# Kernel optimization log

Measured on AMD Instinct MI355X. Metric: run time of the kernel, lower is better.

The kernel has to match this reference:

```python
import jax, jax.numpy as jnp
import numpy as np

N, M, D = 131072, 512, 128  # points, codebook size, feature dim


def setup_inputs() -> dict:
    key = jax.random.key(0)
    k1, k2 = jax.random.split(key)
    X = jax.random.normal(k1, (N, D), dtype=jnp.float32)
    samples = jax.random.normal(k2, (M, D), dtype=jnp.float32)
    return {"X": X, "samples": samples}


def reference(X, samples):
    # Pairwise L2 distance: sum((x - s)^2, axis=-1) ** (1/2), vectorized via
    # for p=2, without materializing an [N, M, D] tensor).
    x2 = jnp.sum(X * X, axis=1, keepdims=True)              # [N, 1]
    s2 = jnp.sum(samples * samples, axis=1)[None, :]        # [1, M]
    d2 = x2 + s2 - 2.0 * (X @ samples.T)                    # [N, M]
    m_dis = jnp.sqrt(jnp.maximum(d2, 0.0))                  # [N, M]
    # soft=True branch: softmax over axis=0 (across points), as in the original.
    return jax.nn.softmax(-m_dis, axis=0)
```

## Files before the change

kernel.cpp:

```cpp
#include <hip/hip_runtime.h>
#include <hip/hip_bf16.h>

#define NPTS 131072
#define MCB  512
#define DIM  128
#define NRB  (NPTS/128)
#define NCBK (MCB/128)
#define NBLK (NRB*NCBK)

typedef __attribute__((ext_vector_type(4))) float  f32x4;
typedef __attribute__((ext_vector_type(8))) __bf16 bf16x8;
typedef unsigned short u16;
typedef unsigned int   u32;

__device__ __forceinline__ u32 swz(u32 p) { return p ^ (((p >> 8) & 7u) << 4); }

__global__ __launch_bounds__(256) void convert_rows(const float* __restrict__ in,
                                                    u16* __restrict__ outb,
                                                    float* __restrict__ sq,
                                                    int nrows) {
  int wv = threadIdx.x >> 6, ln = threadIdx.x & 63;
  int half = ln >> 5, li = ln & 31;
  int npairs = nrows >> 1;
  for (int pr = blockIdx.x * 4 + wv; pr < npairs; pr += gridDim.x * 4) {
    int row = pr * 2 + half;
    const float4 v = *(const float4*)(in + (size_t)row * DIM + li * 4);
    __hip_bfloat16 b0 = __float2bfloat16(v.x);
    __hip_bfloat16 b1 = __float2bfloat16(v.y);
    __hip_bfloat16 b2 = __float2bfloat16(v.z);
    __hip_bfloat16 b3 = __float2bfloat16(v.w);
    ushort4 o;
    o.x = *(const u16*)&b0; o.y = *(const u16*)&b1;
    o.z = *(const u16*)&b2; o.w = *(const u16*)&b3;
    *(ushort4*)(outb + (size_t)row * DIM + li * 4) = o;
    float f0 = __bfloat162float(b0), f1 = __bfloat162float(b1);
    float f2 = __bfloat162float(b2), f3 = __bfloat162float(b3);
    float s = f0 * f0 + f1 * f1 + f2 * f2 + f3 * f3;
    s += __shfl_xor(s, 1); s += __shfl_xor(s, 2); s += __shfl_xor(s, 4);
    s += __shfl_xor(s, 8); s += __shfl_xor(s, 16);
    if (li == 0) sq[row] = s;
  }
}

template <int WRITE>
__global__ __launch_bounds__(256, 3) void gemm_pass(const u16* __restrict__ Xb,
                                                    const u16* __restrict__ Sb,
                                                    const float* __restrict__ x2,
                                                    const float* __restrict__ s2,
                                                    const float* __restrict__ invs,
                                                    float* __restrict__ outp) {
  __shared__ u16 Bt[128 * DIM];
  __shared__ float lx2[128], ls2[128], lscale[128];
  __shared__ float colsum2[4][64];

  int t = threadIdx.x, wv = t >> 6, ln = t & 63;
  u32 h = blockIdx.x;
  u32 l = (h & 7u) * (NBLK / 8) + (h >> 3);
  u32 rb = l >> 2, cb = l & 3u;
  u32 n0 = rb * 128, m0 = cb * 128;

  const char* Bg = (const char*)(Sb + (size_t)m0 * DIM);
#pragma unroll
  for (int i = 0; i < 8; i++) {
    u32 lb = (u32)(i * 4 + wv) * 1024u;
    u32 go = swz(lb + (u32)ln * 16u);
    __builtin_amdgcn_global_load_lds((const __attribute__((address_space(1))) void*)(Bg + go),
                                     (__attribute__((address_space(3))) void*)((char*)Bt + lb),
                                     16, 0, 0);
  }

  int wr = wv >> 1, wc = wv & 1;
  int rbw = wr * 64, cbw = wc * 64;
  int lr = ln & 15, lg = ln >> 4;

  bf16x8 af[4][4];
  const u16* Abase = Xb + (size_t)(n0 + rbw) * DIM;
#pragma unroll
  for (int i = 0; i < 4; i++)
#pragma unroll
    for (int kk = 0; kk < 4; kk++)
      af[i][kk] = *(const bf16x8*)(Abase + (i * 16 + lr) * DIM + kk * 32 + lg * 8);

  if (t < 128) {
    lx2[t] = x2[n0 + t];
    ls2[t] = s2[m0 + t];
    if (WRITE) lscale[t] = invs[m0 + t];
  }
  __syncthreads();

  f32x4 acc[4][4];
#pragma unroll
  for (int i = 0; i < 4; i++)
#pragma unroll
    for (int j = 0; j < 4; j++) acc[i][j] = (f32x4){0.f, 0.f, 0.f, 0.f};

#pragma unroll
  for (int kk = 0; kk < 4; kk++) {
    bf16x8 bfr[4];
#pragma unroll
    for (int j = 0; j < 4; j++)
      bfr[j] = *(const bf16x8*)((const char*)Bt +
               swz((u32)((cbw + j * 16 + lr) * 256 + kk * 64 + lg * 16)));
#pragma unroll
    for (int i = 0; i < 4; i++)
#pragma unroll
      for (int j = 0; j < 4; j++) {
        if (WRITE)
          acc[i][j] = __builtin_amdgcn_mfma_f32_16x16x32_bf16(bfr[j], af[i][kk], acc[i][j], 0, 0, 0);
        else
          acc[i][j] = __builtin_amdgcn_mfma_f32_16x16x32_bf16(af[i][kk], bfr[j], acc[i][j], 0, 0, 0);
      }
  }

  if (WRITE) {
#pragma unroll
    for (int i = 0; i < 4; i++) {
      int n = rbw + i * 16 + lr;
      float xx = lx2[n];
      float* orow = outp + (size_t)(n0 + n) * MCB + m0;
#pragma unroll
      for (int j = 0; j < 4; j++) {
        int mb = cbw + j * 16 + lg * 4;
        f32x4 v;
#pragma unroll
        for (int r = 0; r < 4; r++) {
          float d2 = xx + ls2[mb + r] - 2.f * acc[i][j][r];
          d2 = fmaxf(d2, 0.f);
          float e = __expf(-__fsqrt_rn(d2));
          v[r] = e * lscale[mb + r];
        }
        __builtin_nontemporal_store(v, (f32x4*)(orow + mb));
      }
    }
  } else {
    float csum[4] = {0.f, 0.f, 0.f, 0.f};
#pragma unroll
    for (int i = 0; i < 4; i++) {
#pragma unroll
      for (int j = 0; j < 4; j++) {
        int m = cbw + j * 16 + lr;
        float ss = ls2[m];
#pragma unroll
        for (int r = 0; r < 4; r++) {
          int n = rbw + i * 16 + lg * 4 + r;
          float d2 = lx2[n] + ss - 2.f * acc[i][j][r];
          d2 = fmaxf(d2, 0.f);
          csum[j] += __expf(-__fsqrt_rn(d2));
        }
      }
    }
#pragma unroll
    for (int j = 0; j < 4; j++) {
      float v = csum[j];
      v += __shfl_xor(v, 16);
      v += __shfl_xor(v, 32);
      if (ln < 16) colsum2[wv][j * 16 + ln] = v;
    }
    __syncthreads();
    if (t < 128) {
      int wcf = t >> 6, lc = t & 63;
      outp[(size_t)rb * MCB + m0 + t] = colsum2[wcf][lc] + colsum2[wcf + 2][lc];
    }
  }
}

__global__ __launch_bounds__(256) void reduce_cols(const float* __restrict__ partial,
                                                   float* __restrict__ invs) {
  int m = blockIdx.x, t = threadIdx.x;
  float s = 0.f;
  for (int k = t; k < NRB; k += 256) s += partial[(size_t)k * MCB + m];
  s += __shfl_xor(s, 1);  s += __shfl_xor(s, 2);  s += __shfl_xor(s, 4);
  s += __shfl_xor(s, 8);  s += __shfl_xor(s, 16); s += __shfl_xor(s, 32);
  __shared__ float w4[4];
  if ((t & 63) == 0) w4[t >> 6] = s;
  __syncthreads();
  if (t == 0) invs[m] = 1.0f / (w4[0] + w4[1] + w4[2] + w4[3]);
}

extern "C" void kernel_launch(void* const* d_in, const int* in_sizes, int n_in,
                              void* d_out, int out_size, void* d_ws, size_t ws_size,
                              hipStream_t stream) {
  const float* X = (const float*)d_in[0];
  const float* S = (const float*)d_in[1];
  float* out = (float*)d_out;
  char* ws = (char*)d_ws;

  u16*   Xb      = (u16*)ws;
  u16*   Sb      = (u16*)(ws + 33554432);
  float* x2      = (float*)(ws + 33685504);
  float* s2      = (float*)(ws + 34209792);
  float* invs    = (float*)(ws + 34211840);
  float* partial = (float*)(ws + 34213888);

  convert_rows<<<2048, 256, 0, stream>>>(X, Xb, x2, NPTS);
  convert_rows<<<64, 256, 0, stream>>>(S, Sb, s2, MCB);
  gemm_pass<0><<<NBLK, 256, 0, stream>>>(Xb, Sb, x2, s2, invs, partial);
  reduce_cols<<<MCB, 256, 0, stream>>>(partial, invs);
  gemm_pass<1><<<NBLK, 256, 0, stream>>>(Xb, Sb, x2, s2, invs, out);
}
```

Baseline: 398.3 us.

## Fuse X conversion into pass1 and loop codebook tiles per row block

Folds the X fp32-to-bf16 conversion and row-norm computation into the first GEMM pass, so each block converts its own 128 rows and then reuses them from registers. Each block now iterates over all four 128-column codebook tiles instead of launching one block per tile. This cuts the number of blocks and avoids reloading the A fragments per tile. B fragments now come straight from global/L2 rather than from swizzled LDS, and reduce_cols handles 8 columns per block for coalesced reads. The risks are lower parallelism (1024 blocks), longer per-block serial work, and uncached B loads.

New measurement: 426.6 us. +7.1%, slower.

```diff
diff --git a/kernel.cpp b/kernel.cpp
--- a/kernel.cpp
+++ b/kernel.cpp
@@ -4,16 +4,12 @@
 #define NPTS 131072
 #define MCB  512
 #define DIM  128
-#define NRB  (NPTS/128)
-#define NCBK (MCB/128)
-#define NBLK (NRB*NCBK)
+#define NRB  1024
 
 typedef __attribute__((ext_vector_type(4))) float  f32x4;
 typedef __attribute__((ext_vector_type(8))) __bf16 bf16x8;
 typedef unsigned short u16;
 typedef unsigned int   u32;
-
-__device__ __forceinline__ u32 swz(u32 p) { return p ^ (((p >> 8) & 7u) << 4); }
 
 __global__ __launch_bounds__(256) void convert_rows(const float* __restrict__ in,
                                                     u16* __restrict__ outb,
@@ -42,113 +38,97 @@
   }
 }
 
-template <int WRITE>
-__global__ __launch_bounds__(256, 3) void gemm_pass(const u16* __restrict__ Xb,
-                                                    const u16* __restrict__ Sb,
-                                                    const float* __restrict__ x2,
-                                                    const float* __restrict__ s2,
-                                                    const float* __restrict__ invs,
-                                                    float* __restrict__ outp) {
-  __shared__ u16 Bt[128 * DIM];
-  __shared__ float lx2[128], ls2[128], lscale[128];
+__global__ __launch_bounds__(256, 2) void pass1(const float* __restrict__ X,
+                                                const u16* __restrict__ Sb,
+                                                const float* __restrict__ s2,
+                                                u16* __restrict__ Xb,
+                                                float* __restrict__ x2,
+                                                float* __restrict__ partial) {
   __shared__ float colsum2[4][64];
-
   int t = threadIdx.x, wv = t >> 6, ln = t & 63;
   u32 h = blockIdx.x;
-  u32 l = (h & 7u) * (NBLK / 8) + (h >> 3);
-  u32 rb = l >> 2, cb = l & 3u;
-  u32 n0 = rb * 128, m0 = cb * 128;
-
-  const char* Bg = (const char*)(Sb + (size_t)m0 * DIM);
-#pragma unroll
-  for (int i = 0; i < 8; i++) {
-    u32 lb = (u32)(i * 4 + wv) * 1024u;
-    u32 go = swz(lb + (u32)ln * 16u);
-    __builtin_amdgcn_global_load_lds((const __attribute__((address_space(1))) void*)(Bg + go),
-                                     (__attribute__((address_space(3))) void*)((char*)Bt + lb),
-                                     16, 0, 0);
-  }
+  u32 rb = (h & 7u) * (NRB / 8) + (h >> 3);
+  u32 n0 = rb * 128;
+
+  {
+    int half = ln >> 5, li = ln & 31;
+    const float* Xblk = X + (size_t)n0 * DIM;
+    u16* Xbblk = Xb + (size_t)n0 * DIM;
+#pragma unroll
+    for (int it = 0; it < 16; ++it) {
+      int row = (it * 4 + wv) * 2 + half;
+      const float4 v = *(const float4*)(Xblk + (size_t)row * DIM + li * 4);
+      __hip_bfloat16 b0 = __float2bfloat16(v.x);
+      __hip_bfloat16 b1 = __float2bfloat16(v.y);
+      __hip_bfloat16 b2 = __float2bfloat16(v.z);
+      __hip_bfloat16 b3 = __float2bfloat16(v.w);
+      ushort4 o;
+      o.x = *(const u16*)&b0; o.y = *(const u16*)&b1;
+      o.z = *(const u16*)&b2; o.w = *(const u16*)&b3;
+      *(ushort4*)(Xbblk + (size_t)row * DIM + li * 4) = o;
+      float f0 = __bfloat162float(b0), f1 = __bfloat162float(b1);
+      float f2 = __bfloat162float(b2), f3 = __bfloat162float(b3);
+      float s = f0 * f0 + f1 * f1 + f2 * f2 + f3 * f3;
+      s += __shfl_xor(s, 1); s += __shfl_xor(s, 2); s += __shfl_xor(s, 4);
+      s += __shfl_xor(s, 8); s += __shfl_xor(s, 16);
+      if (li == 0) x2[n0 + row] = s;
+    }
+  }
+  __syncthreads();
 
   int wr = wv >> 1, wc = wv & 1;
   int rbw = wr * 64, cbw = wc * 64;
   int lr = ln & 15, lg = ln >> 4;
 
   bf16x8 af[4][4];
-  const u16* Abase = Xb + (size_t)(n0 + rbw) * DIM;
+  const u16* Ab = Xb + (size_t)(n0 + rbw) * DIM;
 #pragma unroll
   for (int i = 0; i < 4; i++)
 #pragma unroll
     for (int kk = 0; kk < 4; kk++)
-      af[i][kk] = *(const bf16x8*)(Abase + (i * 16 + lr) * DIM + kk * 32 + lg * 8);
-
-  if (t < 128) {
-    lx2[t] = x2[n0 + t];
-    ls2[t] = s2[m0 + t];
-    if (WRITE) lscale[t] = invs[m0 + t];
-  }
-  __syncthreads();
-
-  f32x4 acc[4][4];
+      af[i][kk] = *(const bf16x8*)(Ab + (i * 16 + lr) * DIM + kk * 32 + lg * 8);
+
+  f32x4 lxv[4];
 #pragma unroll
   for (int i = 0; i < 4; i++)
-#pragma unroll
-    for (int j = 0; j < 4; j++) acc[i][j] = (f32x4){0.f, 0.f, 0.f, 0.f};
-
-#pragma unroll
-  for (int kk = 0; kk < 4; kk++) {
-    bf16x8 bfr[4];
-#pragma unroll
-    for (int j = 0; j < 4; j++)
-      bfr[j] = *(const bf16x8*)((const char*)Bt +
-               swz((u32)((cbw + j * 16 + lr) * 256 + kk * 64 + lg * 16)));
+    lxv[i] = *(const f32x4*)(x2 + n0 + rbw + i * 16 + lg * 4);
+
+#pragma unroll
+  for (int cb = 0; cb < 4; ++cb) {
+    int m0c = cb * 128;
+    f32x4 acc[4][4];
 #pragma unroll
     for (int i = 0; i < 4; i++)
 #pragma unroll
-      for (int j = 0; j < 4; j++) {
-        if (WRITE)
-          acc[i][j] = __builtin_amdgcn_mfma_f32_16x16x32_bf16(bfr[j], af[i][kk], acc[i][j], 0, 0, 0);
-        else
-          acc[i][j] = __builtin_amdgcn_mfma_f32_16x16x32_bf16(af[i][kk], bfr[j], acc[i][j], 0, 0, 0);
-      }
-  }
-
-  if (WRITE) {
-#pragma unroll
-    for (int i = 0; i < 4; i++) {
-      int n = rbw + i * 16 + lr;
-      float xx = lx2[n];
-      float* orow = outp + (size_t)(n0 + n) * MCB + m0;
-#pragma unroll
-      for (int j = 0; j < 4; j++) {
-        int mb = cbw + j * 16 + lg * 4;
-        f32x4 v;
+      for (int j = 0; j < 4; j++) acc[i][j] = (f32x4){0.f, 0.f, 0.f, 0.f};
+
+#pragma unroll
+    for (int kk = 0; kk < 4; kk++) {
+      bf16x8 bb[4];
+#pragma unroll
+      for (int j = 0; j < 4; j++)
+        bb[j] = *(const bf16x8*)(Sb + (size_t)(m0c + cbw + j * 16 + lr) * DIM + kk * 32 + lg * 8);
+#pragma unroll
+      for (int i = 0; i < 4; i++)
+#pragma unroll
+        for (int j = 0; j < 4; j++)
+          acc[i][j] = __builtin_amdgcn_mfma_f32_16x16x32_bf16(af[i][kk], bb[j], acc[i][j], 0, 0, 0);
+    }
+
+    float s2v[4];
+#pragma unroll
+    for (int j = 0; j < 4; j++) s2v[j] = s2[m0c + cbw + j * 16 + lr];
+    float csum[4] = {0.f, 0.f, 0.f, 0.f};
+#pragma unroll
+    for (int i = 0; i < 4; i++)
+#pragma unroll
+      for (int j = 0; j < 4; j++)
 #pragma unroll
         for (int r = 0; r < 4; r++) {
-          float d2 = xx + ls2[mb + r] - 2.f * acc[i][j][r];
-          d2 = fmaxf(d2, 0.f);
-          float e = __expf(-__fsqrt_rn(d2));
-          v[r] = e * lscale[mb + r];
-        }
-        __builtin_nontemporal_store(v, (f32x4*)(orow + mb));
-      }
-    }
-  } else {
-    float csum[4] = {0.f, 0.f, 0.f, 0.f};
-#pragma unroll
-    for (int i = 0; i < 4; i++) {
-#pragma unroll
-      for (int j = 0; j < 4; j++) {
-        int m = cbw + j * 16 + lr;
-        float ss = ls2[m];
-#pragma unroll
-        for (int r = 0; r < 4; r++) {
-          int n = rbw + i * 16 + lg * 4 + r;
-          float d2 = lx2[n] + ss - 2.f * acc[i][j][r];
+          float d2 = lxv[i][r] + s2v[j] - 2.f * acc[i][j][r];
           d2 = fmaxf(d2, 0.f);
           csum[j] += __expf(-__fsqrt_rn(d2));
         }
-      }
-    }
 #pragma unroll
     for (int j = 0; j < 4; j++) {
       float v = csum[j];
@@ -159,22 +139,97 @@
     __syncthreads();
     if (t < 128) {
       int wcf = t >> 6, lc = t & 63;
-      outp[(size_t)rb * MCB + m0 + t] = colsum2[wcf][lc] + colsum2[wcf + 2][lc];
-    }
+      partial[(size_t)rb * MCB + m0c + t] = colsum2[wcf][lc] + colsum2[wcf + 2][lc];
+    }
+    __syncthreads();
   }
 }
 
 __global__ __launch_bounds__(256) void reduce_cols(const float* __restrict__ partial,
                                                    float* __restrict__ invs) {
-  int m = blockIdx.x, t = threadIdx.x;
+  int b = blockIdx.x, t = threadIdx.x, ln = t & 63, wv = t >> 6;
+  int m = b * 8 + (t & 7);
   float s = 0.f;
-  for (int k = t; k < NRB; k += 256) s += partial[(size_t)k * MCB + m];
-  s += __shfl_xor(s, 1);  s += __shfl_xor(s, 2);  s += __shfl_xor(s, 4);
-  s += __shfl_xor(s, 8);  s += __shfl_xor(s, 16); s += __shfl_xor(s, 32);
-  __shared__ float w4[4];
-  if ((t & 63) == 0) w4[t >> 6] = s;
+  for (int k = t >> 3; k < NRB; k += 32) s += partial[(size_t)k * MCB + m];
+  s += __shfl_xor(s, 8); s += __shfl_xor(s, 16); s += __shfl_xor(s, 32);
+  __shared__ float red[4][8];
+  if (ln < 8) red[wv][ln] = s;
   __syncthreads();
-  if (t == 0) invs[m] = 1.0f / (w4[0] + w4[1] + w4[2] + w4[3]);
+  if (t < 8) invs[b * 8 + t] = 1.0f / (red[0][t] + red[1][t] + red[2][t] + red[3][t]);
+}
+
+__global__ __launch_bounds__(256, 2) void pass2(const u16* __restrict__ Xb,
+                                                const u16* __restrict__ Sb,
+                                                const float* __restrict__ x2,
+                                                const float* __restrict__ s2,
+                                                const float* __restrict__ invs,
+                                                float* __restrict__ out) {
+  int t = threadIdx.x, wv = t >> 6, ln = t & 63;
+  u32 h = blockIdx.x;
+  u32 rb = (h & 7u) * (NRB / 8) + (h >> 3);
+  u32 n0 = rb * 128;
+
+  int wr = wv >> 1, wc = wv & 1;
+  int rbw = wr * 64, cbw = wc * 64;
+  int lr = ln & 15, lg = ln >> 4;
+
+  bf16x8 af[4][4];
+  const u16* Ab = Xb + (size_t)(n0 + rbw) * DIM;
+#pragma unroll
+  for (int i = 0; i < 4; i++)
+#pragma unroll
+    for (int kk = 0; kk < 4; kk++)
+      af[i][kk] = *(const bf16x8*)(Ab + (i * 16 + lr) * DIM + kk * 32 + lg * 8);
+
+  float xx[4];
+#pragma unroll
+  for (int i = 0; i < 4; i++) xx[i] = x2[n0 + rbw + i * 16 + lr];
+
+#pragma unroll
+  for (int cb = 0; cb < 4; ++cb) {
+    int m0c = cb * 128;
+    f32x4 acc[4][4];
+#pragma unroll
+    for (int i = 0; i < 4; i++)
+#pragma unroll
+      for (int j = 0; j < 4; j++) acc[i][j] = (f32x4){0.f, 0.f, 0.f, 0.f};
+
+#pragma unroll
+    for (int kk = 0; kk < 4; kk++) {
+      bf16x8 bb[4];
+#pragma unroll
+      for (int j = 0; j < 4; j++)
+        bb[j] = *(const bf16x8*)(Sb + (size_t)(m0c + cbw + j * 16 + lr) * DIM + kk * 32 + lg * 8);
+#pragma unroll
+      for (int i = 0; i < 4; i++)
+#pragma unroll
+        for (int j = 0; j < 4; j++)
+          acc[i][j] = __builtin_amdgcn_mfma_f32_16x16x32_bf16(bb[j], af[i][kk], acc[i][j], 0, 0, 0);
+    }
+
+    f32x4 ls2v[4], lscv[4];
+#pragma unroll
+    for (int j = 0; j < 4; j++) {
+      ls2v[j] = *(const f32x4*)(s2  + m0c + cbw + j * 16 + lg * 4);
+      lscv[j] = *(const f32x4*)(invs + m0c + cbw + j * 16 + lg * 4);
+    }
+#pragma unroll
+    for (int i = 0; i < 4; i++) {
+      float xxi = xx[i];
+      float* orow = out + (size_t)(n0 + rbw + i * 16 + lr) * MCB + m0c;
+#pragma unroll
+      for (int j = 0; j < 4; j++) {
+        f32x4 v;
+#pragma unroll
+        for (int r = 0; r < 4; r++) {
+          float d2 = xxi + ls2v[j][r] - 2.f * acc[i][j][r];
+          d2 = fmaxf(d2, 0.f);
+          v[r] = __expf(-__fsqrt_rn(d2)) * lscv[j][r];
+        }
+        __builtin_nontemporal_store(v, (f32x4*)(orow + cbw + j * 16 + lg * 4));
+      }
+    }
+  }
 }
 
 extern "C" void kernel_launch(void* const* d_in, const int* in_sizes, int n_in,
@@ -192,9 +247,8 @@
   float* invs    = (float*)(ws + 34211840);
   float* partial = (float*)(ws + 34213888);
 
-  convert_rows<<<2048, 256, 0, stream>>>(X, Xb, x2, NPTS);
   convert_rows<<<64, 256, 0, stream>>>(S, Sb, s2, MCB);
-  gemm_pass<0><<<NBLK, 256, 0, stream>>>(Xb, Sb, x2, s2, invs, partial);
-  reduce_cols<<<MCB, 256, 0, stream>>>(partial, invs);
-  gemm_pass<1><<<NBLK, 256, 0, stream>>>(Xb, Sb, x2, s2, invs, out);
-}
+  pass1<<<NRB, 256, 0, stream>>>(X, Sb, s2, Xb, x2, partial);
+  reduce_cols<<<64, 256, 0, stream>>>(partial, invs);
+  pass2<<<NRB, 256, 0, stream>>>(Xb, Sb, x2, s2, invs, out);
+}
```

## Stage A tile in LDS via async loads, vectorize epilogue, coalesce column reduce

Applied to the files above, without the earlier changes.

The X tile is now staged into swizzled LDS with global_load_lds alongside the codebook tile, instead of each wave loading its 64 rows straight from global memory into registers. Fragments are read from LDS per k-step, which lowers register pressure. The occupancy hint drops from 3 to 2 because LDS use doubles to about 64KB per block. The write epilogue preloads ls2 and scale as float4 vectors, and reduce_cols now handles 8 columns per block so its reads are more coalesced, with fewer blocks launched.

Measured after the change: 397.9 us. About the same (-0.1%).

```diff
diff --git a/kernel.cpp b/kernel.cpp
--- a/kernel.cpp
+++ b/kernel.cpp
@@ -43,14 +43,15 @@
 }
 
 template <int WRITE>
-__global__ __launch_bounds__(256, 3) void gemm_pass(const u16* __restrict__ Xb,
+__global__ __launch_bounds__(256, 2) void gemm_pass(const u16* __restrict__ Xb,
                                                     const u16* __restrict__ Sb,
                                                     const float* __restrict__ x2,
                                                     const float* __restrict__ s2,
                                                     const float* __restrict__ invs,
                                                     float* __restrict__ outp) {
+  __shared__ u16 At[128 * DIM];
   __shared__ u16 Bt[128 * DIM];
-  __shared__ float lx2[128], ls2[128], lscale[128];
+  __shared__ alignas(16) float lx2[128], ls2[128], lscale[128];
   __shared__ float colsum2[4][64];
 
   int t = threadIdx.x, wv = t >> 6, ln = t & 63;
@@ -59,28 +60,19 @@
   u32 rb = l >> 2, cb = l & 3u;
   u32 n0 = rb * 128, m0 = cb * 128;
 
+  const char* Ag = (const char*)(Xb + (size_t)n0 * DIM);
   const char* Bg = (const char*)(Sb + (size_t)m0 * DIM);
 #pragma unroll
   for (int i = 0; i < 8; i++) {
     u32 lb = (u32)(i * 4 + wv) * 1024u;
     u32 go = swz(lb + (u32)ln * 16u);
+    __builtin_amdgcn_global_load_lds((const __attribute__((address_space(1))) void*)(Ag + go),
+                                     (__attribute__((address_space(3))) void*)((char*)At + lb),
+                                     16, 0, 0);
     __builtin_amdgcn_global_load_lds((const __attribute__((address_space(1))) void*)(Bg + go),
                                      (__attribute__((address_space(3))) void*)((char*)Bt + lb),
                                      16, 0, 0);
   }
-
-  int wr = wv >> 1, wc = wv & 1;
-  int rbw = wr * 64, cbw = wc * 64;
-  int lr = ln & 15, lg = ln >> 4;
-
-  bf16x8 af[4][4];
-  const u16* Abase = Xb + (size_t)(n0 + rbw) * DIM;
-#pragma unroll
-  for (int i = 0; i < 4; i++)
-#pragma unroll
-    for (int kk = 0; kk < 4; kk++)
-      af[i][kk] = *(const bf16x8*)(Abase + (i * 16 + lr) * DIM + kk * 32 + lg * 8);
-
   if (t < 128) {
     lx2[t] = x2[n0 + t];
     ls2[t] = s2[m0 + t];
@@ -88,6 +80,10 @@
   }
   __syncthreads();
 
+  int wr = wv >> 1, wc = wv & 1;
+  int rbw = wr * 64, cbw = wc * 64;
+  int lr = ln & 15, lg = ln >> 4;
+
   f32x4 acc[4][4];
 #pragma unroll
   for (int i = 0; i < 4; i++)
@@ -96,7 +92,11 @@
 
 #pragma unroll
   for (int kk = 0; kk < 4; kk++) {
-    bf16x8 bfr[4];
+    bf16x8 af[4], bfr[4];
+#pragma unroll
+    for (int i = 0; i < 4; i++)
+      af[i] = *(const bf16x8*)((const char*)At +
+               swz((u32)((rbw + i * 16 + lr) * 256 + kk * 64 + lg * 16)));
 #pragma unroll
     for (int j = 0; j < 4; j++)
       bfr[j] = *(const bf16x8*)((const char*)Bt +
@@ -106,13 +106,19 @@
 #pragma unroll
       for (int j = 0; j < 4; j++) {
         if (WRITE)
-          acc[i][j] = __builtin_amdgcn_mfma_f32_16x16x32_bf16(bfr[j], af[i][kk], acc[i][j], 0, 0, 0);
+          acc[i][j] = __builtin_amdgcn_mfma_f32_16x16x32_bf16(bfr[j], af[i], acc[i][j], 0, 0, 0);
         else
-          acc[i][j] = __builtin_amdgcn_mfma_f32_16x16x32_bf16(af[i][kk], bfr[j], acc[i][j], 0, 0, 0);
+          acc[i][j] = __builtin_amdgcn_mfma_f32_16x16x32_bf16(af[i], bfr[j], acc[i][j], 0, 0, 0);
       }
   }
 
   if (WRITE) {
+    f32x4 ls2v[4], lscv[4];
+#pragma unroll
+    for (int j = 0; j < 4; j++) {
+      ls2v[j] = *(const f32x4*)(&ls2[cbw + j * 16 + lg * 4]);
+      lscv[j] = *(const f32x4*)(&lscale[cbw + j * 16 + lg * 4]);
+    }
 #pragma unroll
     for (int i = 0; i < 4; i++) {
       int n = rbw + i * 16 + lr;
@@ -120,16 +126,14 @@
       float* orow = outp + (size_t)(n0 + n) * MCB + m0;
 #pragma unroll
       for (int j = 0; j < 4; j++) {
-        int mb = cbw + j * 16 + lg * 4;
         f32x4 v;
 #pragma unroll
         for (int r = 0; r < 4; r++) {
-          float d2 = xx + ls2[mb + r] - 2.f * acc[i][j][r];
+          float d2 = xx + ls2v[j][r] - 2.f * acc[i][j][r];
           d2 = fmaxf(d2, 0.f);
-          float e = __expf(-__fsqrt_rn(d2));
-          v[r] = e * lscale[mb + r];
+          v[r] = __expf(-__fsqrt_rn(d2)) * lscv[j][r];
         }
-        __builtin_nontemporal_store(v, (f32x4*)(orow + mb));
+        __builtin_nontemporal_store(v, (f32x4*)(orow + cbw + j * 16 + lg * 4));
       }
     }
   } else {
@@ -166,15 +170,15 @@
 
 __global__ __launch_bounds__(256) void reduce_cols(const float* __restrict__ partial,
                                                    float* __restrict__ invs) {
-  int m = blockIdx.x, t = threadIdx.x;
+  int b = blockIdx.x, t = threadIdx.x, ln = t & 63, wv = t >> 6;
+  int m = b * 8 + (t & 7);
   float s = 0.f;
-  for (int k = t; k < NRB; k += 256) s += partial[(size_t)k * MCB + m];
-  s += __shfl_xor(s, 1);  s += __shfl_xor(s, 2);  s += __shfl_xor(s, 4);
-  s += __shfl_xor(s, 8);  s += __shfl_xor(s, 16); s += __shfl_xor(s, 32);
-  __shared__ float w4[4];
-  if ((t & 63) == 0) w4[t >> 6] = s;
+  for (int k = t >> 3; k < NRB; k += 32) s += partial[(size_t)k * MCB + m];
+  s += __shfl_xor(s, 8); s += __shfl_xor(s, 16); s += __shfl_xor(s, 32);
+  __shared__ float red[4][8];
+  if (ln < 8) red[wv][ln] = s;
   __syncthreads();
-  if (t == 0) invs[m] = 1.0f / (w4[0] + w4[1] + w4[2] + w4[3]);
+  if (t < 8) invs[b * 8 + t] = 1.0f / (red[0][t] + red[1][t] + red[2][t] + red[3][t]);
 }
 
 extern "C" void kernel_launch(void* const* d_in, const int* in_sizes, int n_in,
@@ -195,6 +199,6 @@
   convert_rows<<<2048, 256, 0, stream>>>(X, Xb, x2, NPTS);
   convert_rows<<<64, 256, 0, stream>>>(S, Sb, s2, MCB);
   gemm_pass<0><<<NBLK, 256, 0, stream>>>(Xb, Sb, x2, s2, invs, partial);
-  reduce_cols<<<MCB, 256, 0, stream>>>(partial, invs);
+  reduce_cols<<<64, 256, 0, stream>>>(partial, invs);
   gemm_pass<1><<<NBLK, 256, 0, stream>>>(Xb, Sb, x2, s2, invs, out);
 }
```
